# Kernel optimization log

Measured on AMD Instinct MI355X. Metric: run time of the kernel, lower is better.

## Reference

```python
import jax, jax.numpy as jnp
import numpy as np

B, S, D = 2, 2048, 2048
H, KVH = 32, 8
HD = D // H          # 64
N_REP = H // KVH     # 4
NEG = -1e9


def setup_inputs() -> dict:
    key = jax.random.key(0)
    ks = jax.random.split(key, 5)
    x = jax.random.normal(ks[0], (B, S, D), dtype=jnp.float32)
    std = 0.02
    wq = jax.random.normal(ks[1], (H * HD, D), dtype=jnp.float32) * std
    wk = jax.random.normal(ks[2], (KVH * HD, D), dtype=jnp.float32) * std
    wv = jax.random.normal(ks[3], (KVH * HD, D), dtype=jnp.float32) * std
    wo = jax.random.normal(ks[4], (D, H * HD), dtype=jnp.float32) * std
    # RoPE tables: (S, HD//2)
    inv_freq = 1.0 / (10000.0 ** (np.arange(0, HD, 2, dtype=np.float32) / HD))
    t = np.arange(S, dtype=np.float32)
    freqs = np.outer(t, inv_freq)
    freqs_cos = jnp.asarray(np.cos(freqs))
    freqs_sin = jnp.asarray(np.sin(freqs))
    # additive causal mask [1,1,S,S]
    causal = np.tril(np.ones((S, S), dtype=bool))
    mask = jnp.asarray(np.where(causal, 0.0, NEG).astype(np.float32))[None, None]
    return {"x": x, "wq": wq, "wk": wk, "wv": wv, "wo": wo,
            "freqs_cos": freqs_cos, "freqs_sin": freqs_sin, "mask": mask}


def _apply_rope(t, cos, sin):
    # t: [B,S,nh,HD]; cos/sin: [S, HD//2]
    tr = t.reshape(t.shape[:-1] + (HD // 2, 2))
    r, i = tr[..., 0], tr[..., 1]
    c = cos[None, :, None, :]
    s = sin[None, :, None, :]
    out_r = r * c - i * s
    out_i = r * s + i * c
    return jnp.stack([out_r, out_i], axis=-1).reshape(t.shape)


def reference(x, wq, wk, wv, wo, freqs_cos, freqs_sin, mask):
    b, s, _ = x.shape
    q = (x @ wq.T).reshape(b, s, H, HD)
    k = (x @ wk.T).reshape(b, s, KVH, HD)
    v = (x @ wv.T).reshape(b, s, KVH, HD)
    q = _apply_rope(q, freqs_cos, freqs_sin)
    k = _apply_rope(k, freqs_cos, freqs_sin)
    # repeat_kv (GQA expansion) then move heads forward: [B,H,S,HD]
    k = jnp.repeat(k, N_REP, axis=2)
    v = jnp.repeat(v, N_REP, axis=2)
    q = q.transpose(0, 2, 1, 3)
    k = k.transpose(0, 2, 1, 3)
    v = v.transpose(0, 2, 1, 3)
    scale = 1.0 / jnp.sqrt(jnp.float32(HD))
    scores = jnp.einsum("bhqd,bhkd->bhqk", q, k) * scale + mask[:, :, :s, :s]
    attn = jax.nn.softmax(scores, axis=-1)
    out = jnp.einsum("bhqk,bhkd->bhqd", attn, v)
    out = out.transpose(0, 2, 1, 3).reshape(b, s, H * HD)
    return out @ wo.T
```

## Files before the change

kernel.cpp:

```cpp
#include <hip/hip_runtime.h>
#include <hip/hip_bf16.h>
#include <stdint.h>


#define NEG_BIG (-1e9f)
#define SCALE_LOG2 0.18033688011112042f
#define DEFER_THR 10.0f

typedef __bf16 bf16x8 __attribute__((ext_vector_type(8)));
typedef float f32x4 __attribute__((ext_vector_type(4)));
typedef float f32x16 __attribute__((ext_vector_type(16)));
typedef uint16_t u16x8 __attribute__((ext_vector_type(8)));
typedef uint32_t u32x4 __attribute__((ext_vector_type(4)));

__device__ inline uint16_t f2bf(float x) {
    __hip_bfloat16 h = __float2bfloat16(x);
    return __builtin_bit_cast(uint16_t, h);
}
__device__ inline float bf2f(uint16_t u) {
    uint32_t t = (uint32_t)u << 16;
    return __builtin_bit_cast(float, t);
}

__device__ inline void async_cp16(const void* g, void* l) {
    __builtin_amdgcn_global_load_lds(
        (const __attribute__((address_space(1))) uint32_t*)g,
        (__attribute__((address_space(3))) uint32_t*)l,
        16 , 0 , 0 );
}

__global__ void cvt4(const float* __restrict__ in, uint16_t* __restrict__ out, int n4) {
    int i = blockIdx.x * blockDim.x + threadIdx.x;
    if (i >= n4) return;
    const float4 v = ((const float4*)in)[i];
    ushort4 o;
    o.x = f2bf(v.x); o.y = f2bf(v.y); o.z = f2bf(v.z); o.w = f2bf(v.w);
    ((ushort4*)out)[i] = o;
}

__global__ void build_wqkv(const float* __restrict__ wq, const float* __restrict__ wk,
                           const float* __restrict__ wv, uint16_t* __restrict__ out) {
    int i = blockIdx.x * blockDim.x + threadIdx.x;
    if (i >= (3072 * 2048) / 4) return;
    int e = i * 4;
    int row = e >> 11;
    int col = e & 2047;
    const float* src = (row < 2048) ? (wq + (long)row * 2048 + col)
                     : (row < 2560) ? (wk + (long)(row - 2048) * 2048 + col)
                                    : (wv + (long)(row - 2560) * 2048 + col);
    const float4 v = *(const float4*)src;
    ushort4 o;
    o.x = f2bf(v.x); o.y = f2bf(v.y); o.z = f2bf(v.z); o.w = f2bf(v.w);
    ((ushort4*)(out + e))[0] = o;
}

template <int BN, int OUT_BF16>
__global__ __launch_bounds__(512) void gemm256(const uint16_t* __restrict__ A,
                                               const uint16_t* __restrict__ Bw,
                                               void* __restrict__ Cout,
                                               int M, int N, int K) {
    constexpr int WN = BN / 4;
    constexpr int NF = WN / 16;
    constexpr int BROUNDS = BN / 64;

    __shared__ __align__(16) uint16_t As[2][256 * 64];
    __shared__ __align__(16) uint16_t Bs[2][BN * 64];

    const int tid = threadIdx.x;
    const int l = tid & 63;
    const int w = tid >> 6;
    const int wmi = w >> 2;
    const int wni = w & 3;
    const int c = l & 15, g = l >> 4;
    const long row0 = (long)blockIdx.x * 256;
    const long col0 = (long)blockIdx.y * BN;

    f32x4 acc[8][NF] = {};

    auto STAGE = [&](int buf, int t) {
        const long k0 = (long)t * 64;
#pragma unroll
        for (int rr = 0; rr < 4; ++rr) {
            const int e = rr * 512 + tid;
            const int r = e >> 3;
            const int gs = (e & 7) ^ (r & 7);
            async_cp16(A + (row0 + r) * (long)K + k0 + gs * 8, &As[buf][e * 8]);
        }
#pragma unroll
        for (int rr = 0; rr < BROUNDS; ++rr) {
            const int e = rr * 512 + tid;
            const int r = e >> 3;
            const int gs = (e & 7) ^ (r & 7);
            async_cp16(Bw + (col0 + r) * (long)K + k0 + gs * 8, &Bs[buf][e * 8]);
        }
    };

    STAGE(0, 0);
    __syncthreads();

    const int nt = K / 64;
    for (int t = 0; t < nt; ++t) {
        const int cur = t & 1;
        if (t + 1 < nt) STAGE(cur ^ 1, t + 1);

#pragma unroll
        for (int kk = 0; kk < 2; ++kk) {
            bf16x8 bF[NF];
#pragma unroll
            for (int n = 0; n < NF; ++n) {
                const int rb = wni * WN + n * 16 + c;
                const int sp = ((kk * 4 + g) ^ (c & 7));
                bF[n] = *(const bf16x8*)&Bs[cur][rb * 64 + sp * 8];
            }
#pragma unroll
            for (int mh = 0; mh < 2; ++mh) {
                bf16x8 aF[4];
#pragma unroll
                for (int mm = 0; mm < 4; ++mm) {
                    const int ra = wmi * 128 + (mh * 4 + mm) * 16 + c;
                    const int sp = ((kk * 4 + g) ^ (c & 7));
                    aF[mm] = *(const bf16x8*)&As[cur][ra * 64 + sp * 8];
                }
                __builtin_amdgcn_s_setprio(1);
#pragma unroll
                for (int mm = 0; mm < 4; ++mm)
#pragma unroll
                    for (int n = 0; n < NF; ++n)
                        acc[mh * 4 + mm][n] = __builtin_amdgcn_mfma_f32_16x16x32_bf16(
                            aF[mm], bF[n], acc[mh * 4 + mm][n], 0, 0, 0);
                __builtin_amdgcn_s_setprio(0);
            }
        }
        if (t + 1 < nt) __syncthreads();
    }

#pragma unroll
    for (int m = 0; m < 8; ++m) {
        const long rg = row0 + wmi * 128 + m * 16 + g * 4;
#pragma unroll
        for (int n = 0; n < NF; ++n) {
            const long cg = col0 + wni * WN + n * 16 + c;
#pragma unroll
            for (int r = 0; r < 4; ++r) {
                float v = acc[m][n][r];
                if (OUT_BF16)
                    ((uint16_t*)Cout)[(rg + r) * (long)N + cg] = f2bf(v);
                else
                    ((float*)Cout)[(rg + r) * (long)N + cg] = v;
            }
        }
    }
}

__global__ void rope_q(uint16_t* __restrict__ qkv,
                       const float* __restrict__ cosT,
                       const float* __restrict__ sinT) {
    int idx = blockIdx.x * blockDim.x + threadIdx.x;
    if (idx >= 4096 * 1024) return;
    int m = idx >> 10;
    int j = idx & 1023;
    int s = m & 2047;
    int d2 = j & 31;
    float cc = cosT[s * 32 + d2];
    float ss = sinT[s * 32 + d2];
    uint32_t* p = (uint32_t*)(qkv + (long)m * 3072 + 2 * j);
    uint32_t v = *p;
    float re = bf2f((uint16_t)(v & 0xffffu));
    float im = bf2f((uint16_t)(v >> 16));
    float orr = (re * cc - im * ss) * SCALE_LOG2;
    float oi  = (re * ss + im * cc) * SCALE_LOG2;
    *p = (uint32_t)f2bf(orr) | ((uint32_t)f2bf(oi) << 16);
}

__global__ void pack_kv(const uint16_t* __restrict__ qkv,
                        const float* __restrict__ cosT,
                        const float* __restrict__ sinT,
                        uint16_t* __restrict__ Kpk,
                        uint16_t* __restrict__ Vpk) {
    const int gw = (blockIdx.x * blockDim.x + threadIdx.x) >> 6;
    const int l = threadIdx.x & 63;
    const int lq = l & 31, hi = l >> 5;
    if (gw < 4096) {
        const int wid = gw;
        const int s = wid & 3;
        const int tile = (wid >> 2) & 63;
        const int bk = wid >> 8;
        const int b = bk >> 3, kvh = bk & 7;
        const int key = 32 * tile + lq;
        const uint16_t* src = qkv + (long)(b * 2048 + key) * 3072
                            + 2048 + kvh * 64 + 16 * s + 8 * hi;
        u16x8 v = *(const u16x8*)src;
        const int d2b = 8 * s + 4 * hi;
        u16x8 o;
#pragma unroll
        for (int p = 0; p < 4; ++p) {
            const float cc = cosT[key * 32 + d2b + p];
            const float ss = sinT[key * 32 + d2b + p];
            const float re = bf2f(v[2 * p]);
            const float im = bf2f(v[2 * p + 1]);
            o[2 * p]     = f2bf(re * cc - im * ss);
            o[2 * p + 1] = f2bf(re * ss + im * cc);
        }
        *(u16x8*)(Kpk + (((long)(bk * 64 + tile) * 4 + s) * 64 + l) * 8) = o;
    } else {
        const int wid = gw - 4096;
        const int s2 = wid & 1;
        const int nd = (wid >> 1) & 1;
        const int tile = (wid >> 2) & 63;
        const int bk = wid >> 8;
        const int b = bk >> 3, kvh = bk & 7;
        const int key0 = 32 * tile + 16 * s2 + 8 * hi;
        const uint16_t* src = qkv + (long)(b * 2048 + key0) * 3072
                            + 2560 + kvh * 64 + nd * 32 + lq;
        u16x8 v;
#pragma unroll
        for (int jj = 0; jj < 8; ++jj) v[jj] = src[(long)jj * 3072];
        *(u16x8*)(Vpk + ((((long)(bk * 64 + tile) * 2 + nd) * 2 + s2) * 64 + l) * 8) = v;
    }
}

__device__ inline void pack_pf(const float pr[16], int hi, bf16x8 pf[2]) {
    uint32_t wds[8], xw[8];
#pragma unroll
    for (int m = 0; m < 8; ++m)
        wds[m] = (uint32_t)f2bf(pr[2 * m]) | ((uint32_t)f2bf(pr[2 * m + 1]) << 16);
#pragma unroll
    for (int m = 0; m < 8; ++m)
        xw[m] = (uint32_t)__shfl_xor((int)wds[m], 32);
#pragma unroll
    for (int s = 0; s < 2; ++s) {
        u32x4 pk;
        pk[0] = hi ? xw[4 * s + 2] : wds[4 * s + 0];
        pk[1] = hi ? xw[4 * s + 3] : wds[4 * s + 1];
        pk[2] = hi ? wds[4 * s + 2] : xw[4 * s + 0];
        pk[3] = hi ? wds[4 * s + 3] : xw[4 * s + 1];
        pf[s] = __builtin_bit_cast(bf16x8, pk);
    }
}

__global__ __launch_bounds__(128) void attn_fwd(const uint16_t* __restrict__ qkv,
                                                const uint16_t* __restrict__ Kpk,
                                                const uint16_t* __restrict__ Vpk,
                                                uint16_t* __restrict__ outb) {
    const int bid = blockIdx.x;
    const int bhp = bid & 31;
    const int j = 63 - (bid >> 5);
    const int t0 = threadIdx.x;
    const int l = t0 & 63, ww = t0 >> 6;
    const int gh = 2 * bhp + ww;
    const int b = gh >> 5, h = gh & 31;
    const int kvh = h >> 2;
    const int bk = b * 8 + kvh;
    const int lq = l & 31, hi = l >> 5;
    const int q = 32 * j + lq;

    const uint16_t* qrow = qkv + (long)(b * 2048 + q) * 3072 + h * 64 + 8 * hi;
    bf16x8 qf[4];
#pragma unroll
    for (int s = 0; s < 4; ++s) qf[s] = *(const bf16x8*)(qrow + 16 * s);

    float m_run = -1e30f, l_run = 0.f;
    f32x16 accO[2] = {};

    const uint16_t* kbase = Kpk + (long)bk * 64 * 2048 + (long)l * 8;
    const uint16_t* vbase = Vpk + (long)bk * 64 * 2048 + (long)l * 8;
    const int nT = (j + 2) >> 1;

    for (int t = 0; t < nT; ++t) {
        bf16x8 kf[2][4];
#pragma unroll
        for (int u = 0; u < 2; ++u)
#pragma unroll
            for (int s = 0; s < 4; ++s)
                kf[u][s] = *(const bf16x8*)(kbase + (long)(2 * t + u) * 2048 + s * 512);

        f32x16 st0 = {}, st1 = {};
        __builtin_amdgcn_s_setprio(1);
#pragma unroll
        for (int s = 0; s < 4; ++s)
            st0 = __builtin_amdgcn_mfma_f32_32x32x16_bf16(kf[0][s], qf[s], st0, 0, 0, 0);
#pragma unroll
        for (int s = 0; s < 4; ++s)
            st1 = __builtin_amdgcn_mfma_f32_32x32x16_bf16(kf[1][s], qf[s], st1, 0, 0, 0);
        __builtin_amdgcn_s_setprio(0);

        bf16x8 vf[2][2][2];
#pragma unroll
        for (int u = 0; u < 2; ++u)
#pragma unroll
            for (int nd = 0; nd < 2; ++nd)
#pragma unroll
                for (int s2 = 0; s2 < 2; ++s2)
                    vf[u][nd][s2] = *(const bf16x8*)(vbase + (long)(2 * t + u) * 2048 + nd * 1024 + s2 * 512);

        if (t == nT - 1) {
            const int tq0 = lq + ((j - 2 * t) << 5) - 4 * hi;
            const int tq1 = tq0 - 32;
#pragma unroll
            for (int r = 0; r < 16; ++r) {
                const int kc = (r & 3) + 8 * (r >> 2);
                if (kc > tq0) st0[r] = NEG_BIG;
                if (kc > tq1) st1[r] = NEG_BIG;
            }
        }

        float mx[16];
#pragma unroll
        for (int r = 0; r < 16; ++r) mx[r] = fmaxf(st0[r], st1[r]);
#pragma unroll
        for (int off = 8; off; off >>= 1)
#pragma unroll
            for (int r = 0; r < 8; ++r)
                if (r < off) mx[r] = fmaxf(mx[r], mx[r + off]);
        const float vm = fmaxf(mx[0], __shfl_xor(mx[0], 32));

        if (!__all(vm - m_run <= DEFER_THR)) {
            const float mnew = fmaxf(m_run, vm);
            const float alpha = __builtin_amdgcn_exp2f(m_run - mnew);
            m_run = mnew;
            l_run *= alpha;
#pragma unroll
            for (int nd = 0; nd < 2; ++nd)
#pragma unroll
                for (int r = 0; r < 16; ++r) accO[nd][r] *= alpha;
        }

        float pr0[16], pr1[16], sm[8];
#pragma unroll
        for (int r = 0; r < 16; ++r) pr0[r] = __builtin_amdgcn_exp2f(st0[r] - m_run);
#pragma unroll
        for (int r = 0; r < 16; ++r) pr1[r] = __builtin_amdgcn_exp2f(st1[r] - m_run);
#pragma unroll
        for (int m = 0; m < 8; ++m)
            sm[m] = (pr0[2 * m] + pr0[2 * m + 1]) + (pr1[2 * m] + pr1[2 * m + 1]);
#pragma unroll
        for (int off = 4; off; off >>= 1)
#pragma unroll
            for (int r = 0; r < 4; ++r)
                if (r < off) sm[r] += sm[r + off];
        l_run += sm[0] + __shfl_xor(sm[0], 32);

        bf16x8 pf0[2], pf1[2];
        pack_pf(pr0, hi, pf0);
        pack_pf(pr1, hi, pf1);

        __builtin_amdgcn_s_setprio(1);
#pragma unroll
        for (int nd = 0; nd < 2; ++nd) {
            accO[nd] = __builtin_amdgcn_mfma_f32_32x32x16_bf16(vf[0][nd][0], pf0[0], accO[nd], 0, 0, 0);
            accO[nd] = __builtin_amdgcn_mfma_f32_32x32x16_bf16(vf[0][nd][1], pf0[1], accO[nd], 0, 0, 0);
            accO[nd] = __builtin_amdgcn_mfma_f32_32x32x16_bf16(vf[1][nd][0], pf1[0], accO[nd], 0, 0, 0);
            accO[nd] = __builtin_amdgcn_mfma_f32_32x32x16_bf16(vf[1][nd][1], pf1[1], accO[nd], 0, 0, 0);
        }
        __builtin_amdgcn_s_setprio(0);
    }

    const float invl = 1.0f / l_run;
    uint16_t* orow = outb + (long)(b * 2048 + q) * 2048 + h * 64 + 4 * hi;
#pragma unroll
    for (int nd = 0; nd < 2; ++nd)
#pragma unroll
        for (int m = 0; m < 4; ++m) {
            ushort4 o;
            o.x = f2bf(accO[nd][4 * m + 0] * invl);
            o.y = f2bf(accO[nd][4 * m + 1] * invl);
            o.z = f2bf(accO[nd][4 * m + 2] * invl);
            o.w = f2bf(accO[nd][4 * m + 3] * invl);
            *(ushort4*)(orow + nd * 32 + 8 * m) = o;
        }
}

extern "C" void kernel_launch(void* const* d_in, const int* in_sizes, int n_in,
                              void* d_out, int out_size, void* d_ws, size_t ws_size,
                              hipStream_t stream) {
    const float* x    = (const float*)d_in[0];
    const float* wq   = (const float*)d_in[1];
    const float* wk   = (const float*)d_in[2];
    const float* wv   = (const float*)d_in[3];
    const float* wo   = (const float*)d_in[4];
    const float* fcos = (const float*)d_in[5];
    const float* fsin = (const float*)d_in[6];
    float* out = (float*)d_out;

    uint8_t* ws = (uint8_t*)d_ws;
    const size_t MiB = 1048576;
    uint16_t* x_bf   = (uint16_t*)(ws);
    uint16_t* w_bf   = (uint16_t*)(ws + 16 * MiB);
    uint16_t* qkv_bf = (uint16_t*)(ws + 28 * MiB);
    uint16_t* att_bf = x_bf;
    uint16_t* Kpk    = (uint16_t*)(ws + 16 * MiB);
    uint16_t* Vpk    = (uint16_t*)(ws + 20 * MiB);
    uint16_t* wo_bf  = (uint16_t*)(ws + 16 * MiB);

    cvt4<<<(2097152 + 255) / 256, 256, 0, stream>>>(x, x_bf, 2097152);
    build_wqkv<<<(1572864 + 255) / 256, 256, 0, stream>>>(wq, wk, wv, w_bf);

    gemm256<192, 1><<<dim3(16, 16), 512, 0, stream>>>(x_bf, w_bf, qkv_bf, 4096, 3072, 2048);

    rope_q<<<16384, 256, 0, stream>>>(qkv_bf, fcos, fsin);
    pack_kv<<<2048, 256, 0, stream>>>(qkv_bf, fcos, fsin, Kpk, Vpk);

    attn_fwd<<<2048, 128, 0, stream>>>(qkv_bf, Kpk, Vpk, att_bf);

    cvt4<<<(1048576 + 255) / 256, 256, 0, stream>>>(wo, wo_bf, 1048576);
    gemm256<128, 0><<<dim3(16, 16), 512, 0, stream>>>(att_bf, wo_bf, out, 4096, 2048, 2048);
}
```

Measured before the change: 212.4 us.

## Fuse Q RoPE into attention, use permlane32 swap, remap GEMM block order

Removes the separate rope_q kernel and applies RoPE plus the softmax scale to Q while loading it inside attn_fwd. This drops one launch and a full read-modify-write pass over the Q part of qkv. The P-fragment packing now uses v_permlane32_swap_b32 inline asm in place of eight shuffles and selects. GEMM launches switch to a 1D grid with a custom tile mapping, likely aimed at L2 locality. Each attention block now recomputes RoPE for its Q tile and loads cos/sin itself.

```diff
diff --git a/kernel.cpp b/kernel.cpp
--- a/kernel.cpp
+++ b/kernel.cpp
@@ -66,14 +66,18 @@
     __shared__ __align__(16) uint16_t As[2][256 * 64];
     __shared__ __align__(16) uint16_t Bs[2][BN * 64];
 
+    const int n0 = blockIdx.x;
+    const int colt = 2 * (n0 & 7) + ((n0 >> 3) >> 4);
+    const int rowt = (n0 >> 3) & 15;
+    const long row0 = (long)rowt * 256;
+    const long col0 = (long)colt * BN;
+
     const int tid = threadIdx.x;
     const int l = tid & 63;
     const int w = tid >> 6;
     const int wmi = w >> 2;
     const int wni = w & 3;
     const int c = l & 15, g = l >> 4;
-    const long row0 = (long)blockIdx.x * 256;
-    const long col0 = (long)blockIdx.y * BN;
 
     f32x4 acc[8][NF] = {};
 
@@ -150,26 +154,6 @@
             }
         }
     }
-}
-
-__global__ void rope_q(uint16_t* __restrict__ qkv,
-                       const float* __restrict__ cosT,
-                       const float* __restrict__ sinT) {
-    int idx = blockIdx.x * blockDim.x + threadIdx.x;
-    if (idx >= 4096 * 1024) return;
-    int m = idx >> 10;
-    int j = idx & 1023;
-    int s = m & 2047;
-    int d2 = j & 31;
-    float cc = cosT[s * 32 + d2];
-    float ss = sinT[s * 32 + d2];
-    uint32_t* p = (uint32_t*)(qkv + (long)m * 3072 + 2 * j);
-    uint32_t v = *p;
-    float re = bf2f((uint16_t)(v & 0xffffu));
-    float im = bf2f((uint16_t)(v >> 16));
-    float orr = (re * cc - im * ss) * SCALE_LOG2;
-    float oi  = (re * ss + im * cc) * SCALE_LOG2;
-    *p = (uint32_t)f2bf(orr) | ((uint32_t)f2bf(oi) << 16);
 }
 
 __global__ void pack_kv(const uint16_t* __restrict__ qkv,
@@ -219,26 +203,24 @@
     }
 }
 
-__device__ inline void pack_pf(const float pr[16], int hi, bf16x8 pf[2]) {
-    uint32_t wds[8], xw[8];
+__device__ inline void pack_pf(const float pr[16], bf16x8 pf[2]) {
+    uint32_t wds[8];
 #pragma unroll
     for (int m = 0; m < 8; ++m)
         wds[m] = (uint32_t)f2bf(pr[2 * m]) | ((uint32_t)f2bf(pr[2 * m + 1]) << 16);
-#pragma unroll
-    for (int m = 0; m < 8; ++m)
-        xw[m] = (uint32_t)__shfl_xor((int)wds[m], 32);
-#pragma unroll
-    for (int s = 0; s < 2; ++s) {
-        u32x4 pk;
-        pk[0] = hi ? xw[4 * s + 2] : wds[4 * s + 0];
-        pk[1] = hi ? xw[4 * s + 3] : wds[4 * s + 1];
-        pk[2] = hi ? wds[4 * s + 2] : xw[4 * s + 0];
-        pk[3] = hi ? wds[4 * s + 3] : xw[4 * s + 1];
-        pf[s] = __builtin_bit_cast(bf16x8, pk);
-    }
+    asm volatile("v_permlane32_swap_b32 %0, %1" : "+v"(wds[0]), "+v"(wds[2]));
+    asm volatile("v_permlane32_swap_b32 %0, %1" : "+v"(wds[1]), "+v"(wds[3]));
+    asm volatile("v_permlane32_swap_b32 %0, %1" : "+v"(wds[4]), "+v"(wds[6]));
+    asm volatile("v_permlane32_swap_b32 %0, %1" : "+v"(wds[5]), "+v"(wds[7]));
+    u32x4 pk0 = {wds[0], wds[1], wds[2], wds[3]};
+    u32x4 pk1 = {wds[4], wds[5], wds[6], wds[7]};
+    pf[0] = __builtin_bit_cast(bf16x8, pk0);
+    pf[1] = __builtin_bit_cast(bf16x8, pk1);
 }
 
 __global__ __launch_bounds__(128) void attn_fwd(const uint16_t* __restrict__ qkv,
+                                                const float* __restrict__ cosT,
+                                                const float* __restrict__ sinT,
                                                 const uint16_t* __restrict__ Kpk,
                                                 const uint16_t* __restrict__ Vpk,
                                                 uint16_t* __restrict__ outb) {
@@ -257,7 +239,21 @@
     const uint16_t* qrow = qkv + (long)(b * 2048 + q) * 3072 + h * 64 + 8 * hi;
     bf16x8 qf[4];
 #pragma unroll
-    for (int s = 0; s < 4; ++s) qf[s] = *(const bf16x8*)(qrow + 16 * s);
+    for (int s = 0; s < 4; ++s) {
+        const u16x8 v = *(const u16x8*)(qrow + 16 * s);
+        const int d2b = 8 * s + 4 * hi;
+        u16x8 o;
+#pragma unroll
+        for (int p = 0; p < 4; ++p) {
+            const float cc = cosT[q * 32 + d2b + p];
+            const float ss = sinT[q * 32 + d2b + p];
+            const float re = bf2f(v[2 * p]);
+            const float im = bf2f(v[2 * p + 1]);
+            o[2 * p]     = f2bf((re * cc - im * ss) * SCALE_LOG2);
+            o[2 * p + 1] = f2bf((re * ss + im * cc) * SCALE_LOG2);
+        }
+        qf[s] = __builtin_bit_cast(bf16x8, o);
+    }
 
     float m_run = -1e30f, l_run = 0.f;
     f32x16 accO[2] = {};
@@ -341,8 +337,8 @@
         l_run += sm[0] + __shfl_xor(sm[0], 32);
 
         bf16x8 pf0[2], pf1[2];
-        pack_pf(pr0, hi, pf0);
-        pack_pf(pr1, hi, pf1);
+        pack_pf(pr0, pf0);
+        pack_pf(pr1, pf1);
 
         __builtin_amdgcn_s_setprio(1);
 #pragma unroll
@@ -395,13 +391,12 @@
     cvt4<<<(2097152 + 255) / 256, 256, 0, stream>>>(x, x_bf, 2097152);
     build_wqkv<<<(1572864 + 255) / 256, 256, 0, stream>>>(wq, wk, wv, w_bf);
 
-    gemm256<192, 1><<<dim3(16, 16), 512, 0, stream>>>(x_bf, w_bf, qkv_bf, 4096, 3072, 2048);
-
-    rope_q<<<16384, 256, 0, stream>>>(qkv_bf, fcos, fsin);
+    gemm256<192, 1><<<256, 512, 0, stream>>>(x_bf, w_bf, qkv_bf, 4096, 3072, 2048);
+
     pack_kv<<<2048, 256, 0, stream>>>(qkv_bf, fcos, fsin, Kpk, Vpk);
 
-    attn_fwd<<<2048, 128, 0, stream>>>(qkv_bf, Kpk, Vpk, att_bf);
+    attn_fwd<<<2048, 128, 0, stream>>>(qkv_bf, fcos, fsin, Kpk, Vpk, att_bf);
 
     cvt4<<<(1048576 + 255) / 256, 256, 0, stream>>>(wo, wo_bf, 1048576);
-    gemm256<128, 0><<<dim3(16, 16), 512, 0, stream>>>(att_bf, wo_bf, out, 4096, 2048, 2048);
-}
+    gemm256<128, 0><<<256, 512, 0, stream>>>(att_bf, wo_bf, out, 4096, 2048, 2048);
+}
```

Result: faster. 204.0 us (-4.0%).
